# Optimization experiments

Measured on AMD Instinct MI355X. Metric: run time of the kernel, lower is better.

## Reference

```python
import jax, jax.numpy as jnp
import numpy as np

B, S, E, H, A, V = 64, 256, 512, 512, 512, 50000
PAD = 0


def setup_inputs() -> dict:
    key = jax.random.key(0)
    ks = jax.random.split(key, 12)
    src = jax.random.randint(ks[0], (B, S), 0, V)
    src_lens = jax.random.randint(ks[1], (B,), 1, S + 1)
    asp_hidden = jax.random.normal(ks[2], (B, A), jnp.float32)
    embedding = jax.random.normal(ks[3], (V, E), jnp.float32) * 0.02
    embedding = embedding.at[PAD].set(0.0)  # nn.Embedding padding_idx row is zero
    s = 1.0 / np.sqrt(H)
    u = lambda k, shp: jax.random.uniform(k, shp, jnp.float32, -s, s)
    return {
        'src': src, 'src_lens': src_lens, 'asp_hidden': asp_hidden,
        'embedding': embedding,
        'Wx_f': u(ks[4], (E, 3 * H)), 'Wh_f': u(ks[5], (H, 3 * H)),
        'Wa_f': u(ks[6], (A, 3 * H)), 'b_f': u(ks[7], (3 * H,)),
        'Wx_b': u(ks[8], (E, 3 * H)), 'Wh_b': u(ks[9], (H, 3 * H)),
        'Wa_b': u(ks[10], (A, 3 * H)), 'b_b': u(ks[11], (3 * H,)),
    }


def _gru_scan(xg_seq, h0, Wh):
    # xg_seq: [S, B, 3H] = x@Wx + asp@Wa + b (precomputed, time-major)
    def step(h, xg):
        hg = h @ Wh  # [B, 3H]
        xr, xz, xn = jnp.split(xg, 3, axis=-1)
        hr, hz, hn = jnp.split(hg, 3, axis=-1)
        r = jax.nn.sigmoid(xr + hr)
        z = jax.nn.sigmoid(xz + hz)
        n = jnp.tanh(xn + r * hn)
        h = (1.0 - z) * h + z * n
        return h, h
    hT, outs = jax.lax.scan(step, h0, xg_seq)
    return hT, outs  # [B,H], [S,B,H]


def reference(src, src_lens, asp_hidden, embedding,
              Wx_f, Wh_f, Wa_f, b_f, Wx_b, Wh_b, Wa_b, b_b):
    x = embedding[src]                              # [B, S, E]
    batch = src.shape[0]
    h0 = jnp.zeros((batch, Wh_f.shape[0]), x.dtype)  # zero-init state

    def run(xseq, Wx, Wh, Wa, b):
        asp_g = asp_hidden @ Wa + b                 # [B, 3H], aspect-conditioned gate bias
        xg = jnp.einsum('bse,eg->sbg', xseq, Wx) + asp_g[None]
        return _gru_scan(xg, h0, Wh)

    hT_f, out_f = run(x, Wx_f, Wh_f, Wa_f, b_f)
    hT_b, out_b = run(x[:, ::-1], Wx_b, Wh_b, Wa_b, b_b)
    out_b = out_b[::-1]                             # realign reversed direction

    memory_bank = jnp.concatenate([out_f, out_b], -1).transpose(1, 0, 2)  # [B,S,2H]
    # final_state order is [fwd, bwd]; wrapper cats final[-1] (bwd) then final[-2] (fwd)
    encoder_last = jnp.concatenate([hT_b, hT_f], -1)  # [B, 2H]
    return memory_bank, encoder_last
```

## Files before the change

### kernel.cpp

```cpp
#include <hip/hip_runtime.h>
#include <hip/hip_bf16.h>

typedef __bf16 bf16x8 __attribute__((ext_vector_type(8)));
typedef float f32x4 __attribute__((ext_vector_type(4)));
typedef unsigned int u32;
typedef unsigned short u16;

#define NB 64
#define NS 256
#define NE 512
#define NH 512
#define NG 1536
#define NM (NS*NB)

__device__ __forceinline__ float fsig(float x) { return 1.0f/(1.0f + __expf(-x)); }
__device__ __forceinline__ float ftanh(float x) {
  float ax = fabsf(x);
  float t = __expf(-2.0f*ax);
  float r = (1.0f - t)/(1.0f + t);
  return copysignf(r, x);
}

__device__ __forceinline__ void store_u16_wt(void* p, u32 val, int byteoff) {
  switch (byteoff) {
    case 0:    asm volatile("global_store_short %0, %1, off sc0 sc1" :: "v"(p), "v"(val) : "memory"); break;
    case 1024: asm volatile("global_store_short %0, %1, off offset:1024 sc0 sc1" :: "v"(p), "v"(val) : "memory"); break;
    case 2048: asm volatile("global_store_short %0, %1, off offset:2048 sc0 sc1" :: "v"(p), "v"(val) : "memory"); break;
    default:   asm volatile("global_store_short %0, %1, off offset:3072 sc0 sc1" :: "v"(p), "v"(val) : "memory"); break;
  }
}
__device__ __forceinline__ void store_u32_wt(void* p, u32 val) {
  asm volatile("global_store_dword %0, %1, off sc0 sc1" :: "v"(p), "v"(val) : "memory");
}
#define HLOAD(dst, off) \
  asm volatile("global_load_dwordx4 %0, %1, off offset:" off " sc0 sc1" \
               : "=v"(dst) : "v"(hl) : "memory")

__global__ __launch_bounds__(256) void k_gather(const int* __restrict__ src,
                                                const float* __restrict__ emb,
                                                __hip_bfloat16* __restrict__ xsb) {
  int row = blockIdx.x*4 + (threadIdx.x >> 6);
  int lane = threadIdx.x & 63;
  int s = row >> 6, b = row & 63;
  int idx = src[b*NS + s];
  const float* erow = emb + (long)idx*NE + lane*8;
  float4 v0 = *(const float4*)erow;
  float4 v1 = *(const float4*)(erow + 4);
  __hip_bfloat16 tmp[8];
  tmp[0]=__float2bfloat16(v0.x); tmp[1]=__float2bfloat16(v0.y);
  tmp[2]=__float2bfloat16(v0.z); tmp[3]=__float2bfloat16(v0.w);
  tmp[4]=__float2bfloat16(v1.x); tmp[5]=__float2bfloat16(v1.y);
  tmp[6]=__float2bfloat16(v1.z); tmp[7]=__float2bfloat16(v1.w);
  *(uint4*)(xsb + (long)row*NE + lane*8) = *(uint4*)tmp;
}

__global__ __launch_bounds__(256) void k_transpose(const float* i0, const float* i1,
                                                   const float* i2, const float* i3,
                                                   __hip_bfloat16* o0, __hip_bfloat16* o1,
                                                   __hip_bfloat16* o2, __hip_bfloat16* o3) {
  const float* in; __hip_bfloat16* out;
  switch (blockIdx.z) {
    case 0: in=i0; out=o0; break;
    case 1: in=i1; out=o1; break;
    case 2: in=i2; out=o2; break;
    default: in=i3; out=o3; break;
  }
  __shared__ float t[32][33];
  int e0 = blockIdx.x*32, g0 = blockIdx.y*32;
  int r = threadIdx.x >> 5, c = threadIdx.x & 31;
  #pragma unroll
  for (int i=0;i<4;i++) t[r+8*i][c] = in[(long)(e0+r+8*i)*NG + g0+c];
  __syncthreads();
  #pragma unroll
  for (int i=0;i<4;i++) out[(long)(g0+r+8*i)*NE + e0+c] = __float2bfloat16(t[c][r+8*i]);
}

__global__ __launch_bounds__(256) void k_aspg(const float* __restrict__ asp,
     const float* __restrict__ Wa_f, const float* __restrict__ bias_f,
     const float* __restrict__ Wa_b, const float* __restrict__ bias_b,
     float* __restrict__ aspg_f, float* __restrict__ aspg_b) {
  int dir = blockIdx.z;
  const float* Wa  = dir ? Wa_b  : Wa_f;
  const float* bia = dir ? bias_b : bias_f;
  float* outp = dir ? aspg_b : aspg_f;
  int g = blockIdx.x*256 + threadIdx.x;
  int b0 = blockIdx.y*8;
  __shared__ float la[8*512];
  #pragma unroll
  for (int i=0;i<16;i++){ int idx=i*256+threadIdx.x; la[idx] = asp[(long)(b0 + (idx>>9))*512 + (idx&511)]; }
  __syncthreads();
  float bv = bia[g];
  float acc[8];
  #pragma unroll
  for (int bb=0;bb<8;bb++) acc[bb]=bv;
  for (int a=0;a<512;a++){
    float w = Wa[(long)a*NG + g];
    #pragma unroll
    for (int bb=0;bb<8;bb++) acc[bb] += la[bb*512+a]*w;
  }
  #pragma unroll
  for (int bb=0;bb<8;bb++) outp[(long)(b0+bb)*NG + g] = acc[bb];
}

__global__ __launch_bounds__(256,3) void k_xgemm(const __hip_bfloat16* __restrict__ A,
                                                 const __hip_bfloat16* __restrict__ WT,
                                                 __hip_bfloat16* __restrict__ C) {
  __shared__ __hip_bfloat16 sA[128*64];
  __shared__ __hip_bfloat16 sB[64*64];
  const int tid = threadIdx.x;
  const int m0 = blockIdx.y*128, n0 = blockIdx.x*64;
  const int wv = tid>>6, lane = tid&63, l16 = lane&15, lq = lane>>4;
  const int wm = wv>>1, wn = wv&1;
  const int srow = tid>>3, sslot = tid&7;
  f32x4 acc[4][2] = {};
  for (int kt=0; kt<8; ++kt) {
    int k0 = kt*64;
    __syncthreads();
    #pragma unroll
    for (int i=0;i<4;i++){
      int row = i*32 + srow;
      const __hip_bfloat16* src = A + (size_t)(m0+row)*512 + k0 + ((sslot ^ (row&7))*8);
      __builtin_amdgcn_global_load_lds(
        (const __attribute__((address_space(1))) void*)src,
        (__attribute__((address_space(3))) void*)((char*)sA + (i*256 + wv*64)*16), 16, 0, 0);
    }
    #pragma unroll
    for (int i=0;i<2;i++){
      int row = i*32 + srow;
      const __hip_bfloat16* src = WT + (size_t)(n0+row)*512 + k0 + ((sslot ^ (row&7))*8);
      __builtin_amdgcn_global_load_lds(
        (const __attribute__((address_space(1))) void*)src,
        (__attribute__((address_space(3))) void*)((char*)sB + (i*256 + wv*64)*16), 16, 0, 0);
    }
    __syncthreads();
    #pragma unroll
    for (int kk=0; kk<64; kk+=32) {
      bf16x8 af[4]; bf16x8 bfv[2];
      #pragma unroll
      for (int mf=0;mf<4;mf++){
        int row = wm*64 + mf*16 + l16;
        int slot = ((kk>>3) + lq) ^ (row&7);
        af[mf] = *(const bf16x8*)((char*)sA + (row*8 + slot)*16);
      }
      #pragma unroll
      for (int nf=0;nf<2;nf++){
        int row = wn*32 + nf*16 + l16;
        int slot = ((kk>>3) + lq) ^ (row&7);
        bfv[nf] = *(const bf16x8*)((char*)sB + (row*8 + slot)*16);
      }
      #pragma unroll
      for (int mf=0;mf<4;mf++)
        #pragma unroll
        for (int nf=0;nf<2;nf++)
          acc[mf][nf] = __builtin_amdgcn_mfma_f32_16x16x32_bf16(af[mf], bfv[nf], acc[mf][nf], 0,0,0);
    }
  }
  #pragma unroll
  for (int mf=0;mf<4;mf++)
    #pragma unroll
    for (int nf=0;nf<2;nf++)
      #pragma unroll
      for (int r=0;r<4;r++){
        int mrow = m0 + wm*64 + mf*16 + lq*4 + r;
        int col = n0 + wn*32 + nf*16 + l16;
        int gate = col >> 9, cin = col & 511;
        int jwg = cin >> 4, c16 = cin & 15;
        C[((size_t)jwg*NM + mrow)*48 + gate*16 + c16] = __float2bfloat16(acc[mf][nf][r]);
      }
}

__global__ __launch_bounds__(256,1) void k_scan(
   const __hip_bfloat16* __restrict__ xg_f, const __hip_bfloat16* __restrict__ xg_b,
   const __hip_bfloat16* __restrict__ whT_f, const __hip_bfloat16* __restrict__ whT_b,
   const float* __restrict__ aspg_f, const float* __restrict__ aspg_b,
   __hip_bfloat16* __restrict__ hbase, u32* __restrict__ flags,
   float* __restrict__ out)
{
  const int dir = blockIdx.y;
  const int jwg = blockIdx.x;
  const int tid = threadIdx.x;
  const int wm = tid>>6, lane = tid&63, l16 = lane&15, lq = lane>>4;
  const int mrow = wm*16 + l16;
  const __hip_bfloat16* xgd = (dir ? xg_b : xg_f) + (size_t)jwg*NM*48;
  const __hip_bfloat16* whT = dir ? whT_b : whT_f;
  const float* aspg = dir ? aspg_b : aspg_f;
  __hip_bfloat16* hb = hbase + (size_t)dir*2*NB*NH;
  u32* fl = flags + dir*256;

  __shared__ __hip_bfloat16 wl[3*16*512];

  #pragma unroll
  for (int i=0;i<12;i++){
    int cc = i*256 + tid;
    int c = cc>>6, slot = cc&63;
    int gcol = (c>>4)*512 + jwg*16 + (c&15);
    uint4 v = *(const uint4*)(whT + (long)gcol*512 + slot*8);
    *(uint4*)((char*)wl + (c*64 + (slot ^ (c&7)))*16) = v;
  }

  const int jcol = jwg*16 + l16;
  float aspr[3][4];
  float hreg[4] = {0.f,0.f,0.f,0.f};
  #pragma unroll
  for (int g=0; g<3; ++g)
    #pragma unroll
    for (int r=0;r<4;++r){
      int b = wm*16 + lq*4 + r;
      aspr[g][r] = aspg[(long)b*NG + g*512 + jcol];
    }
  __syncthreads();

  u32* fp = fl + ((lane < 32 ? lane : 0)*4 + wm);
  float* out2 = out + (long)NB*NS*1024;

  for (int t=0; t<NS; ++t) {
    int s = dir ? (NS-1-t) : t;
    const __hip_bfloat16* xs = xgd + (size_t)s*NB*48;
    __hip_bfloat16 xr[3][4];
    #pragma unroll
    for (int g=0;g<3;++g)
      #pragma unroll
      for (int r=0;r<4;++r){
        int b = wm*16 + lq*4 + r;
        xr[g][r] = xs[b*48 + g*16 + l16];
      }
    __builtin_amdgcn_sched_barrier(0);
    if (t > 0) {
      const u32 tgt = (u32)t;
      for (;;) {
        u32 f = __hip_atomic_load(fp, __ATOMIC_RELAXED, __HIP_MEMORY_SCOPE_AGENT);
        if (__all((int)(f >= tgt))) break;
      }
    }
    const char* hl = (const char*)(hb + (t&1)*NB*NH) + mrow*1024 + lq*16;
    uint4 hv[16];
    HLOAD(hv[0],  "0");   HLOAD(hv[1],  "64");  HLOAD(hv[2],  "128"); HLOAD(hv[3],  "192");
    HLOAD(hv[4],  "256"); HLOAD(hv[5],  "320"); HLOAD(hv[6],  "384"); HLOAD(hv[7],  "448");
    HLOAD(hv[8],  "512"); HLOAD(hv[9],  "576"); HLOAD(hv[10], "640"); HLOAD(hv[11], "704");
    HLOAD(hv[12], "768"); HLOAD(hv[13], "832"); HLOAD(hv[14], "896"); HLOAD(hv[15], "960");
    asm volatile("s_waitcnt vmcnt(0)" ::: "memory");
    __builtin_amdgcn_sched_barrier(0);
    f32x4 accg[3] = {};
    #pragma unroll
    for (int kc=0;kc<16;++kc){
      bf16x8 af;
      __builtin_memcpy(&af, &hv[kc], 16);
      #pragma unroll
      for (int g=0; g<3; ++g){
        int c = g*16 + l16;
        bf16x8 bfr = *(const bf16x8*)((char*)wl + (c*64 + ((kc*4+lq) ^ (c&7)))*16);
        accg[g] = __builtin_amdgcn_mfma_f32_16x16x32_bf16(af, bfr, accg[g], 0,0,0);
      }
    }
    char* hs = (char*)(hb + ((t+1)&1)*NB*NH) + (size_t)(wm*16 + lq*4)*1024 + jcol*2;
    #pragma unroll
    for (int r=0;r<4;++r){
      float rg = fsig(__bfloat162float(xr[0][r]) + aspr[0][r] + accg[0][r]);
      float zg = fsig(__bfloat162float(xr[1][r]) + aspr[1][r] + accg[1][r]);
      float ng = ftanh(__bfloat162float(xr[2][r]) + aspr[2][r] + rg*accg[2][r]);
      float h = (1.f - zg)*hreg[r] + zg*ng;
      hreg[r] = h;
      __hip_bfloat16 hbf = __float2bfloat16(h);
      u16 bits; __builtin_memcpy(&bits, &hbf, 2);
      store_u16_wt(hs, (u32)bits, r*1024);
    }
    asm volatile("s_waitcnt vmcnt(0)" ::: "memory");
    if (lane == 0)
      store_u32_wt(fl + jwg*4 + wm, (u32)(t+1));
    #pragma unroll
    for (int r=0;r<4;++r){
      int b = wm*16 + lq*4 + r;
      out[((long)b*NS + s)*1024 + dir*512 + jcol] = hreg[r];
    }
  }
  #pragma unroll
  for (int r=0;r<4;++r){
    int b = wm*16 + lq*4 + r;
    out2[(long)b*1024 + (dir ? 0 : 512) + jcol] = hreg[r];
  }
}

extern "C" void kernel_launch(void* const* d_in, const int* in_sizes, int n_in,
                              void* d_out, int out_size, void* d_ws, size_t ws_size,
                              hipStream_t stream) {
  const int*   src  = (const int*)  d_in[0];
  const float* asp  = (const float*)d_in[2];
  const float* emb  = (const float*)d_in[3];
  const float* Wx_f = (const float*)d_in[4];
  const float* Wh_f = (const float*)d_in[5];
  const float* Wa_f = (const float*)d_in[6];
  const float* b_f  = (const float*)d_in[7];
  const float* Wx_b = (const float*)d_in[8];
  const float* Wh_b = (const float*)d_in[9];
  const float* Wa_b = (const float*)d_in[10];
  const float* b_b  = (const float*)d_in[11];

  char* ws = (char*)d_ws;
  size_t o = 0;
  auto alloc = [&](size_t bytes)->char* { char* p = ws + o; o += (bytes + 255) & ~(size_t)255; return p; };
  __hip_bfloat16* xsb    = (__hip_bfloat16*)alloc((size_t)NM*NE*2);
  __hip_bfloat16* wxT_f  = (__hip_bfloat16*)alloc((size_t)NG*NE*2);
  __hip_bfloat16* wxT_b  = (__hip_bfloat16*)alloc((size_t)NG*NE*2);
  __hip_bfloat16* whT_f  = (__hip_bfloat16*)alloc((size_t)NG*NH*2);
  __hip_bfloat16* whT_b  = (__hip_bfloat16*)alloc((size_t)NG*NH*2);
  float*          aspg_f = (float*)alloc((size_t)NB*NG*4);
  float*          aspg_b = (float*)alloc((size_t)NB*NG*4);
  __hip_bfloat16* xg_f   = (__hip_bfloat16*)alloc((size_t)NM*NG*2);
  __hip_bfloat16* xg_b   = (__hip_bfloat16*)alloc((size_t)NM*NG*2);
  __hip_bfloat16* hbuf   = (__hip_bfloat16*)alloc((size_t)2*2*NB*NH*2);
  u32*            flags  = (u32*)alloc((size_t)2*256*4);

  hipMemsetAsync(hbuf, 0, (size_t)2*2*NB*NH*2 + (size_t)2*256*4, stream);

  k_gather<<<dim3(NM/4), 256, 0, stream>>>(src, emb, xsb);
  k_transpose<<<dim3(16,48,4), 256, 0, stream>>>(Wx_f, Wx_b, Wh_f, Wh_b, wxT_f, wxT_b, whT_f, whT_b);
  k_aspg<<<dim3(6,8,2), 256, 0, stream>>>(asp, Wa_f, b_f, Wa_b, b_b, aspg_f, aspg_b);
  k_xgemm<<<dim3(24,128), 256, 0, stream>>>(xsb, wxT_f, xg_f);
  k_xgemm<<<dim3(24,128), 256, 0, stream>>>(xsb, wxT_b, xg_b);
  k_scan<<<dim3(32,2), 256, 0, stream>>>(xg_f, xg_b, whT_f, whT_b, aspg_f, aspg_b,
                                         hbuf, flags, (float*)d_out);
}
```

Before: 1.711 ms.

## Use per-timestep hidden-state buffers so scan reads use normal cached loads

The two ping-pong hidden-state buffers are replaced by one buffer slot per timestep and direction. Each address is then written only once per launch, so the per-step h reads can be ordinary compiler-scheduled vector loads instead of inline-asm loads with sc0 sc1 cache-bypass bits. The recurrent matmul is also skipped at t=0, where h is zero, so only the flags need to be zeroed by the memset. In exchange the workspace grows to about 33 MB of h history, and correctness now relies on no stale cached copies of lines being read after the flag wait.

```diff
diff --git a/kernel.cpp b/kernel.cpp
--- a/kernel.cpp
+++ b/kernel.cpp
@@ -32,9 +32,6 @@
 __device__ __forceinline__ void store_u32_wt(void* p, u32 val) {
   asm volatile("global_store_dword %0, %1, off sc0 sc1" :: "v"(p), "v"(val) : "memory");
 }
-#define HLOAD(dst, off) \
-  asm volatile("global_load_dwordx4 %0, %1, off offset:" off " sc0 sc1" \
-               : "=v"(dst) : "v"(hl) : "memory")
 
 __global__ __launch_bounds__(256) void k_gather(const int* __restrict__ src,
                                                 const float* __restrict__ emb,
@@ -173,7 +170,7 @@
    const __hip_bfloat16* __restrict__ xg_f, const __hip_bfloat16* __restrict__ xg_b,
    const __hip_bfloat16* __restrict__ whT_f, const __hip_bfloat16* __restrict__ whT_b,
    const float* __restrict__ aspg_f, const float* __restrict__ aspg_b,
-   __hip_bfloat16* __restrict__ hbase, u32* __restrict__ flags,
+   __hip_bfloat16* __restrict__ hrot, u32* __restrict__ flags,
    float* __restrict__ out)
 {
   const int dir = blockIdx.y;
@@ -184,7 +181,6 @@
   const __hip_bfloat16* xgd = (dir ? xg_b : xg_f) + (size_t)jwg*NM*48;
   const __hip_bfloat16* whT = dir ? whT_b : whT_f;
   const float* aspg = dir ? aspg_b : aspg_f;
-  __hip_bfloat16* hb = hbase + (size_t)dir*2*NB*NH;
   u32* fl = flags + dir*256;
 
   __shared__ __hip_bfloat16 wl[3*16*512];
@@ -225,34 +221,31 @@
         xr[g][r] = xs[b*48 + g*16 + l16];
       }
     __builtin_amdgcn_sched_barrier(0);
+    f32x4 accg[3] = {};
     if (t > 0) {
       const u32 tgt = (u32)t;
       for (;;) {
         u32 f = __hip_atomic_load(fp, __ATOMIC_RELAXED, __HIP_MEMORY_SCOPE_AGENT);
         if (__all((int)(f >= tgt))) break;
       }
-    }
-    const char* hl = (const char*)(hb + (t&1)*NB*NH) + mrow*1024 + lq*16;
-    uint4 hv[16];
-    HLOAD(hv[0],  "0");   HLOAD(hv[1],  "64");  HLOAD(hv[2],  "128"); HLOAD(hv[3],  "192");
-    HLOAD(hv[4],  "256"); HLOAD(hv[5],  "320"); HLOAD(hv[6],  "384"); HLOAD(hv[7],  "448");
-    HLOAD(hv[8],  "512"); HLOAD(hv[9],  "576"); HLOAD(hv[10], "640"); HLOAD(hv[11], "704");
-    HLOAD(hv[12], "768"); HLOAD(hv[13], "832"); HLOAD(hv[14], "896"); HLOAD(hv[15], "960");
-    asm volatile("s_waitcnt vmcnt(0)" ::: "memory");
-    __builtin_amdgcn_sched_barrier(0);
-    f32x4 accg[3] = {};
-    #pragma unroll
-    for (int kc=0;kc<16;++kc){
-      bf16x8 af;
-      __builtin_memcpy(&af, &hv[kc], 16);
-      #pragma unroll
-      for (int g=0; g<3; ++g){
-        int c = g*16 + l16;
-        bf16x8 bfr = *(const bf16x8*)((char*)wl + (c*64 + ((kc*4+lq) ^ (c&7)))*16);
-        accg[g] = __builtin_amdgcn_mfma_f32_16x16x32_bf16(af, bfr, accg[g], 0,0,0);
-      }
-    }
-    char* hs = (char*)(hb + ((t+1)&1)*NB*NH) + (size_t)(wm*16 + lq*4)*1024 + jcol*2;
+      asm volatile("" ::: "memory");
+      __builtin_amdgcn_sched_barrier(0);
+      const __hip_bfloat16* hin = hrot + ((size_t)(t-1)*2 + dir)*NB*NH;
+      bf16x8 afr[16];
+      #pragma unroll
+      for (int kc=0;kc<16;++kc)
+        afr[kc] = *(const bf16x8*)(hin + (size_t)mrow*NH + kc*32 + lq*8);
+      #pragma unroll
+      for (int kc=0;kc<16;++kc){
+        #pragma unroll
+        for (int g=0; g<3; ++g){
+          int c = g*16 + l16;
+          bf16x8 bfr = *(const bf16x8*)((char*)wl + (c*64 + ((kc*4+lq) ^ (c&7)))*16);
+          accg[g] = __builtin_amdgcn_mfma_f32_16x16x32_bf16(afr[kc], bfr, accg[g], 0,0,0);
+        }
+      }
+    }
+    char* hsto = (char*)(hrot + ((size_t)t*2 + dir)*NB*NH) + (size_t)(wm*16+lq*4)*1024 + jcol*2;
     #pragma unroll
     for (int r=0;r<4;++r){
       float rg = fsig(__bfloat162float(xr[0][r]) + aspr[0][r] + accg[0][r]);
@@ -262,7 +255,7 @@
       hreg[r] = h;
       __hip_bfloat16 hbf = __float2bfloat16(h);
       u16 bits; __builtin_memcpy(&bits, &hbf, 2);
-      store_u16_wt(hs, (u32)bits, r*1024);
+      store_u16_wt(hsto, (u32)bits, r*1024);
     }
     asm volatile("s_waitcnt vmcnt(0)" ::: "memory");
     if (lane == 0)
@@ -307,10 +300,10 @@
   float*          aspg_b = (float*)alloc((size_t)NB*NG*4);
   __hip_bfloat16* xg_f   = (__hip_bfloat16*)alloc((size_t)NM*NG*2);
   __hip_bfloat16* xg_b   = (__hip_bfloat16*)alloc((size_t)NM*NG*2);
-  __hip_bfloat16* hbuf   = (__hip_bfloat16*)alloc((size_t)2*2*NB*NH*2);
+  __hip_bfloat16* hrot   = (__hip_bfloat16*)alloc((size_t)NS*2*NB*NH*2);
   u32*            flags  = (u32*)alloc((size_t)2*256*4);
 
-  hipMemsetAsync(hbuf, 0, (size_t)2*2*NB*NH*2 + (size_t)2*256*4, stream);
+  hipMemsetAsync(flags, 0, (size_t)2*256*4, stream);
 
   k_gather<<<dim3(NM/4), 256, 0, stream>>>(src, emb, xsb);
   k_transpose<<<dim3(16,48,4), 256, 0, stream>>>(Wx_f, Wx_b, Wh_f, Wh_b, wxT_f, wxT_b, whT_f, whT_b);
@@ -318,5 +311,5 @@
   k_xgemm<<<dim3(24,128), 256, 0, stream>>>(xsb, wxT_f, xg_f);
   k_xgemm<<<dim3(24,128), 256, 0, stream>>>(xsb, wxT_b, xg_b);
   k_scan<<<dim3(32,2), 256, 0, stream>>>(xg_f, xg_b, whT_f, whT_b, aspg_f, aspg_b,
-                                         hbuf, flags, (float*)d_out);
-}
+                                         hrot, flags, (float*)d_out);
+}
```

Result: slower. 1.959 ms (+14.4%).

## Issue h chunk loads incrementally as producer flags arrive; fold aspect bias into xgemm

Applied to the files above, without the earlier changes.

The recurrent scan now polls the per-workgroup flags and issues each 64-byte slice of the previous hidden state as soon as both producer workgroups for that slice have published. Previously it waited for all 32 flags before loading anything, so this overlaps memory latency with straggling producers. The aspect-conditioned gate bias is now added in the input-projection GEMM epilogue rather than held in registers and added every scan step. That frees registers and removes adds, but the bias-plus-projection sum is now rounded to bf16 together. The first step also skips the recurrent MFMA, since the initial state is zero.

```diff
diff --git a/kernel.cpp b/kernel.cpp
--- a/kernel.cpp
+++ b/kernel.cpp
@@ -104,6 +104,7 @@
 
 __global__ __launch_bounds__(256,3) void k_xgemm(const __hip_bfloat16* __restrict__ A,
                                                  const __hip_bfloat16* __restrict__ WT,
+                                                 const float* __restrict__ aspg,
                                                  __hip_bfloat16* __restrict__ C) {
   __shared__ __hip_bfloat16 sA[128*64];
   __shared__ __hip_bfloat16 sB[64*64];
@@ -163,16 +164,16 @@
       for (int r=0;r<4;r++){
         int mrow = m0 + wm*64 + mf*16 + lq*4 + r;
         int col = n0 + wn*32 + nf*16 + l16;
+        float v = acc[mf][nf][r] + aspg[(size_t)(mrow & 63)*NG + col];
         int gate = col >> 9, cin = col & 511;
         int jwg = cin >> 4, c16 = cin & 15;
-        C[((size_t)jwg*NM + mrow)*48 + gate*16 + c16] = __float2bfloat16(acc[mf][nf][r]);
+        C[((size_t)jwg*NM + mrow)*48 + gate*16 + c16] = __float2bfloat16(v);
       }
 }
 
 __global__ __launch_bounds__(256,1) void k_scan(
    const __hip_bfloat16* __restrict__ xg_f, const __hip_bfloat16* __restrict__ xg_b,
    const __hip_bfloat16* __restrict__ whT_f, const __hip_bfloat16* __restrict__ whT_b,
-   const float* __restrict__ aspg_f, const float* __restrict__ aspg_b,
    __hip_bfloat16* __restrict__ hbase, u32* __restrict__ flags,
    float* __restrict__ out)
 {
@@ -183,7 +184,6 @@
   const int mrow = wm*16 + l16;
   const __hip_bfloat16* xgd = (dir ? xg_b : xg_f) + (size_t)jwg*NM*48;
   const __hip_bfloat16* whT = dir ? whT_b : whT_f;
-  const float* aspg = dir ? aspg_b : aspg_f;
   __hip_bfloat16* hb = hbase + (size_t)dir*2*NB*NH;
   u32* fl = flags + dir*256;
 
@@ -199,18 +199,10 @@
   }
 
   const int jcol = jwg*16 + l16;
-  float aspr[3][4];
   float hreg[4] = {0.f,0.f,0.f,0.f};
-  #pragma unroll
-  for (int g=0; g<3; ++g)
-    #pragma unroll
-    for (int r=0;r<4;++r){
-      int b = wm*16 + lq*4 + r;
-      aspr[g][r] = aspg[(long)b*NG + g*512 + jcol];
-    }
   __syncthreads();
 
-  u32* fp = fl + ((lane < 32 ? lane : 0)*4 + wm);
+  u32* fp = fl + (lane & 31)*4 + wm;
   float* out2 = out + (long)NB*NS*1024;
 
   for (int t=0; t<NS; ++t) {
@@ -225,39 +217,61 @@
         xr[g][r] = xs[b*48 + g*16 + l16];
       }
     __builtin_amdgcn_sched_barrier(0);
+    f32x4 accg[3] = {};
     if (t > 0) {
       const u32 tgt = (u32)t;
-      for (;;) {
-        u32 f = __hip_atomic_load(fp, __ATOMIC_RELAXED, __HIP_MEMORY_SCOPE_AGENT);
-        if (__all((int)(f >= tgt))) break;
-      }
-    }
-    const char* hl = (const char*)(hb + (t&1)*NB*NH) + mrow*1024 + lq*16;
-    uint4 hv[16];
-    HLOAD(hv[0],  "0");   HLOAD(hv[1],  "64");  HLOAD(hv[2],  "128"); HLOAD(hv[3],  "192");
-    HLOAD(hv[4],  "256"); HLOAD(hv[5],  "320"); HLOAD(hv[6],  "384"); HLOAD(hv[7],  "448");
-    HLOAD(hv[8],  "512"); HLOAD(hv[9],  "576"); HLOAD(hv[10], "640"); HLOAD(hv[11], "704");
-    HLOAD(hv[12], "768"); HLOAD(hv[13], "832"); HLOAD(hv[14], "896"); HLOAD(hv[15], "960");
-    asm volatile("s_waitcnt vmcnt(0)" ::: "memory");
-    __builtin_amdgcn_sched_barrier(0);
-    f32x4 accg[3] = {};
-    #pragma unroll
-    for (int kc=0;kc<16;++kc){
-      bf16x8 af;
-      __builtin_memcpy(&af, &hv[kc], 16);
-      #pragma unroll
-      for (int g=0; g<3; ++g){
-        int c = g*16 + l16;
-        bf16x8 bfr = *(const bf16x8*)((char*)wl + (c*64 + ((kc*4+lq) ^ (c&7)))*16);
-        accg[g] = __builtin_amdgcn_mfma_f32_16x16x32_bf16(af, bfr, accg[g], 0,0,0);
+      const char* hl = (const char*)(hb + (t&1)*NB*NH) + mrow*1024 + lq*16;
+      uint4 hv[16];
+      u32 issued = 0;
+      do {
+        u32 f;
+        asm volatile("global_load_dword %0, %1, off sc0 sc1\n\ts_waitcnt vmcnt(0)"
+                     : "=v"(f) : "v"(fp) : "memory");
+        unsigned long long bal = __ballot((int)(f >= tgt));
+        u32 pr = (u32)(bal & 0xFFFFFFFFull);
+        u32 pairs = pr & (pr >> 1) & 0x55555555u;
+        u32 cm = 0;
+        #pragma unroll
+        for (int kc=0;kc<16;++kc) cm |= ((pairs >> (2*kc)) & 1u) << kc;
+        u32 newc = cm & ~issued;
+        if (newc & 0x0001u) HLOAD(hv[0],  "0");
+        if (newc & 0x0002u) HLOAD(hv[1],  "64");
+        if (newc & 0x0004u) HLOAD(hv[2],  "128");
+        if (newc & 0x0008u) HLOAD(hv[3],  "192");
+        if (newc & 0x0010u) HLOAD(hv[4],  "256");
+        if (newc & 0x0020u) HLOAD(hv[5],  "320");
+        if (newc & 0x0040u) HLOAD(hv[6],  "384");
+        if (newc & 0x0080u) HLOAD(hv[7],  "448");
+        if (newc & 0x0100u) HLOAD(hv[8],  "512");
+        if (newc & 0x0200u) HLOAD(hv[9],  "576");
+        if (newc & 0x0400u) HLOAD(hv[10], "640");
+        if (newc & 0x0800u) HLOAD(hv[11], "704");
+        if (newc & 0x1000u) HLOAD(hv[12], "768");
+        if (newc & 0x2000u) HLOAD(hv[13], "832");
+        if (newc & 0x4000u) HLOAD(hv[14], "896");
+        if (newc & 0x8000u) HLOAD(hv[15], "960");
+        issued |= newc;
+      } while (issued != 0xFFFFu);
+      asm volatile("s_waitcnt vmcnt(0)" ::: "memory");
+      __builtin_amdgcn_sched_barrier(0);
+      #pragma unroll
+      for (int kc=0;kc<16;++kc){
+        bf16x8 af;
+        __builtin_memcpy(&af, &hv[kc], 16);
+        #pragma unroll
+        for (int g=0; g<3; ++g){
+          int c = g*16 + l16;
+          bf16x8 bfr = *(const bf16x8*)((char*)wl + (c*64 + ((kc*4+lq) ^ (c&7)))*16);
+          accg[g] = __builtin_amdgcn_mfma_f32_16x16x32_bf16(af, bfr, accg[g], 0,0,0);
+        }
       }
     }
     char* hs = (char*)(hb + ((t+1)&1)*NB*NH) + (size_t)(wm*16 + lq*4)*1024 + jcol*2;
     #pragma unroll
     for (int r=0;r<4;++r){
-      float rg = fsig(__bfloat162float(xr[0][r]) + aspr[0][r] + accg[0][r]);
-      float zg = fsig(__bfloat162float(xr[1][r]) + aspr[1][r] + accg[1][r]);
-      float ng = ftanh(__bfloat162float(xr[2][r]) + aspr[2][r] + rg*accg[2][r]);
+      float rg = fsig(__bfloat162float(xr[0][r]) + accg[0][r]);
+      float zg = fsig(__bfloat162float(xr[1][r]) + accg[1][r]);
+      float ng = ftanh(__bfloat162float(xr[2][r]) + rg*accg[2][r]);
       float h = (1.f - zg)*hreg[r] + zg*ng;
       hreg[r] = h;
       __hip_bfloat16 hbf = __float2bfloat16(h);
@@ -315,8 +329,7 @@
   k_gather<<<dim3(NM/4), 256, 0, stream>>>(src, emb, xsb);
   k_transpose<<<dim3(16,48,4), 256, 0, stream>>>(Wx_f, Wx_b, Wh_f, Wh_b, wxT_f, wxT_b, whT_f, whT_b);
   k_aspg<<<dim3(6,8,2), 256, 0, stream>>>(asp, Wa_f, b_f, Wa_b, b_b, aspg_f, aspg_b);
-  k_xgemm<<<dim3(24,128), 256, 0, stream>>>(xsb, wxT_f, xg_f);
-  k_xgemm<<<dim3(24,128), 256, 0, stream>>>(xsb, wxT_b, xg_b);
-  k_scan<<<dim3(32,2), 256, 0, stream>>>(xg_f, xg_b, whT_f, whT_b, aspg_f, aspg_b,
-                                         hbuf, flags, (float*)d_out);
-}
+  k_xgemm<<<dim3(24,128), 256, 0, stream>>>(xsb, wxT_f, aspg_f, xg_f);
+  k_xgemm<<<dim3(24,128), 256, 0, stream>>>(xsb, wxT_b, aspg_b, xg_b);
+  k_scan<<<dim3(32,2), 256, 0, stream>>>(xg_f, xg_b, whT_f, whT_b, hbuf, flags, (float*)d_out);
+}
```

Result: no change. 1.693 ms (median of 2 runs) (-1.1%).

## Fold aspect gate bias into x-GEMM, pipeline flag polling, skip step-0 recurrent matmul

Applied to the files above, without the earlier changes.

Adds the aspect-conditioned gate bias into the x-projection GEMM epilogue, so the scan kernel no longer keeps or adds it per step. Flag polling in the scan now uses two overlapping uncached loads, which cuts the round-trip latency of the spin-wait between timesteps. The hidden-state load and recurrent MFMA are skipped at t=0, where h is zero. In exchange the bias is rounded to bf16 together with the x-projection, which adds some precision loss, and the GEMM epilogue gains extra global reads.

```diff
diff --git a/kernel.cpp b/kernel.cpp
--- a/kernel.cpp
+++ b/kernel.cpp
@@ -104,6 +104,7 @@
 
 __global__ __launch_bounds__(256,3) void k_xgemm(const __hip_bfloat16* __restrict__ A,
                                                  const __hip_bfloat16* __restrict__ WT,
+                                                 const float* __restrict__ aspg,
                                                  __hip_bfloat16* __restrict__ C) {
   __shared__ __hip_bfloat16 sA[128*64];
   __shared__ __hip_bfloat16 sB[64*64];
@@ -163,16 +164,16 @@
       for (int r=0;r<4;r++){
         int mrow = m0 + wm*64 + mf*16 + lq*4 + r;
         int col = n0 + wn*32 + nf*16 + l16;
+        float v = acc[mf][nf][r] + aspg[(size_t)(mrow & 63)*NG + col];
         int gate = col >> 9, cin = col & 511;
         int jwg = cin >> 4, c16 = cin & 15;
-        C[((size_t)jwg*NM + mrow)*48 + gate*16 + c16] = __float2bfloat16(acc[mf][nf][r]);
+        C[((size_t)jwg*NM + mrow)*48 + gate*16 + c16] = __float2bfloat16(v);
       }
 }
 
 __global__ __launch_bounds__(256,1) void k_scan(
    const __hip_bfloat16* __restrict__ xg_f, const __hip_bfloat16* __restrict__ xg_b,
    const __hip_bfloat16* __restrict__ whT_f, const __hip_bfloat16* __restrict__ whT_b,
-   const float* __restrict__ aspg_f, const float* __restrict__ aspg_b,
    __hip_bfloat16* __restrict__ hbase, u32* __restrict__ flags,
    float* __restrict__ out)
 {
@@ -183,7 +184,6 @@
   const int mrow = wm*16 + l16;
   const __hip_bfloat16* xgd = (dir ? xg_b : xg_f) + (size_t)jwg*NM*48;
   const __hip_bfloat16* whT = dir ? whT_b : whT_f;
-  const float* aspg = dir ? aspg_b : aspg_f;
   __hip_bfloat16* hb = hbase + (size_t)dir*2*NB*NH;
   u32* fl = flags + dir*256;
 
@@ -199,18 +199,10 @@
   }
 
   const int jcol = jwg*16 + l16;
-  float aspr[3][4];
   float hreg[4] = {0.f,0.f,0.f,0.f};
-  #pragma unroll
-  for (int g=0; g<3; ++g)
-    #pragma unroll
-    for (int r=0;r<4;++r){
-      int b = wm*16 + lq*4 + r;
-      aspr[g][r] = aspg[(long)b*NG + g*512 + jcol];
-    }
   __syncthreads();
 
-  u32* fp = fl + ((lane < 32 ? lane : 0)*4 + wm);
+  u32* fp = fl + (lane & 31)*4 + wm;
   float* out2 = out + (long)NB*NS*1024;
 
   for (int t=0; t<NS; ++t) {
@@ -225,39 +217,47 @@
         xr[g][r] = xs[b*48 + g*16 + l16];
       }
     __builtin_amdgcn_sched_barrier(0);
+    f32x4 accg[3] = {};
     if (t > 0) {
       const u32 tgt = (u32)t;
+      u32 f0, f1;
+      asm volatile("global_load_dword %0, %1, off sc0 sc1" : "=v"(f0) : "v"(fp) : "memory");
       for (;;) {
-        u32 f = __hip_atomic_load(fp, __ATOMIC_RELAXED, __HIP_MEMORY_SCOPE_AGENT);
-        if (__all((int)(f >= tgt))) break;
-      }
-    }
-    const char* hl = (const char*)(hb + (t&1)*NB*NH) + mrow*1024 + lq*16;
-    uint4 hv[16];
-    HLOAD(hv[0],  "0");   HLOAD(hv[1],  "64");  HLOAD(hv[2],  "128"); HLOAD(hv[3],  "192");
-    HLOAD(hv[4],  "256"); HLOAD(hv[5],  "320"); HLOAD(hv[6],  "384"); HLOAD(hv[7],  "448");
-    HLOAD(hv[8],  "512"); HLOAD(hv[9],  "576"); HLOAD(hv[10], "640"); HLOAD(hv[11], "704");
-    HLOAD(hv[12], "768"); HLOAD(hv[13], "832"); HLOAD(hv[14], "896"); HLOAD(hv[15], "960");
-    asm volatile("s_waitcnt vmcnt(0)" ::: "memory");
-    __builtin_amdgcn_sched_barrier(0);
-    f32x4 accg[3] = {};
-    #pragma unroll
-    for (int kc=0;kc<16;++kc){
-      bf16x8 af;
-      __builtin_memcpy(&af, &hv[kc], 16);
-      #pragma unroll
-      for (int g=0; g<3; ++g){
-        int c = g*16 + l16;
-        bf16x8 bfr = *(const bf16x8*)((char*)wl + (c*64 + ((kc*4+lq) ^ (c&7)))*16);
-        accg[g] = __builtin_amdgcn_mfma_f32_16x16x32_bf16(af, bfr, accg[g], 0,0,0);
+        asm volatile("global_load_dword %0, %1, off sc0 sc1" : "=v"(f1) : "v"(fp) : "memory");
+        asm volatile("s_waitcnt vmcnt(1)" ::: "memory");
+        if (__all((int)(f0 >= tgt))) break;
+        asm volatile("global_load_dword %0, %1, off sc0 sc1" : "=v"(f0) : "v"(fp) : "memory");
+        asm volatile("s_waitcnt vmcnt(1)" ::: "memory");
+        if (__all((int)(f1 >= tgt))) break;
+      }
+      asm volatile("s_waitcnt vmcnt(0)" ::: "memory");
+      __builtin_amdgcn_sched_barrier(0);
+      const char* hl = (const char*)(hb + (t&1)*NB*NH) + mrow*1024 + lq*16;
+      uint4 hv[16];
+      HLOAD(hv[0],  "0");   HLOAD(hv[1],  "64");  HLOAD(hv[2],  "128"); HLOAD(hv[3],  "192");
+      HLOAD(hv[4],  "256"); HLOAD(hv[5],  "320"); HLOAD(hv[6],  "384"); HLOAD(hv[7],  "448");
+      HLOAD(hv[8],  "512"); HLOAD(hv[9],  "576"); HLOAD(hv[10], "640"); HLOAD(hv[11], "704");
+      HLOAD(hv[12], "768"); HLOAD(hv[13], "832"); HLOAD(hv[14], "896"); HLOAD(hv[15], "960");
+      asm volatile("s_waitcnt vmcnt(0)" ::: "memory");
+      __builtin_amdgcn_sched_barrier(0);
+      #pragma unroll
+      for (int kc=0;kc<16;++kc){
+        bf16x8 af;
+        __builtin_memcpy(&af, &hv[kc], 16);
+        #pragma unroll
+        for (int g=0; g<3; ++g){
+          int c = g*16 + l16;
+          bf16x8 bfr = *(const bf16x8*)((char*)wl + (c*64 + ((kc*4+lq) ^ (c&7)))*16);
+          accg[g] = __builtin_amdgcn_mfma_f32_16x16x32_bf16(af, bfr, accg[g], 0,0,0);
+        }
       }
     }
     char* hs = (char*)(hb + ((t+1)&1)*NB*NH) + (size_t)(wm*16 + lq*4)*1024 + jcol*2;
     #pragma unroll
     for (int r=0;r<4;++r){
-      float rg = fsig(__bfloat162float(xr[0][r]) + aspr[0][r] + accg[0][r]);
-      float zg = fsig(__bfloat162float(xr[1][r]) + aspr[1][r] + accg[1][r]);
-      float ng = ftanh(__bfloat162float(xr[2][r]) + aspr[2][r] + rg*accg[2][r]);
+      float rg = fsig(__bfloat162float(xr[0][r]) + accg[0][r]);
+      float zg = fsig(__bfloat162float(xr[1][r]) + accg[1][r]);
+      float ng = ftanh(__bfloat162float(xr[2][r]) + rg*accg[2][r]);
       float h = (1.f - zg)*hreg[r] + zg*ng;
       hreg[r] = h;
       __hip_bfloat16 hbf = __float2bfloat16(h);
@@ -315,8 +315,7 @@
   k_gather<<<dim3(NM/4), 256, 0, stream>>>(src, emb, xsb);
   k_transpose<<<dim3(16,48,4), 256, 0, stream>>>(Wx_f, Wx_b, Wh_f, Wh_b, wxT_f, wxT_b, whT_f, whT_b);
   k_aspg<<<dim3(6,8,2), 256, 0, stream>>>(asp, Wa_f, b_f, Wa_b, b_b, aspg_f, aspg_b);
-  k_xgemm<<<dim3(24,128), 256, 0, stream>>>(xsb, wxT_f, xg_f);
-  k_xgemm<<<dim3(24,128), 256, 0, stream>>>(xsb, wxT_b, xg_b);
-  k_scan<<<dim3(32,2), 256, 0, stream>>>(xg_f, xg_b, whT_f, whT_b, aspg_f, aspg_b,
-                                         hbuf, flags, (float*)d_out);
-}
+  k_xgemm<<<dim3(24,128), 256, 0, stream>>>(xsb, wxT_f, aspg_f, xg_f);
+  k_xgemm<<<dim3(24,128), 256, 0, stream>>>(xsb, wxT_b, aspg_b, xg_b);
+  k_scan<<<dim3(32,2), 256, 0, stream>>>(xg_f, xg_b, whT_f, whT_b, hbuf, flags, (float*)d_out);
+}
```

After: 1.914 ms. 1.12x slower.
